# Performance work log

Hardware: AMD Instinct MI355X
Metric: run time of the kernel (lower is better)

Reference implementation:

```python
import jax, jax.numpy as jnp
import numpy as np

B, S, D, N = 8, 4096, 1024, 64
SHIFT_FRAC = 0.5
LN_EPS = 1e-5


def setup_inputs() -> dict:
    key = jax.random.key(0)
    ks = jax.random.split(key, 6)
    x = jax.random.normal(ks[0], (B, S, D), jnp.float32)
    # decay in (-1, 0] so w = exp(decay) in (e^-1, 1] -- stable recurrence
    time_decay = -jax.random.uniform(ks[1], (N,), jnp.float32)
    time_first = 0.1 * jax.random.normal(ks[2], (N,), jnp.float32)
    key_w = jax.random.normal(ks[3], (N, D), jnp.float32) / np.float32(np.sqrt(D))
    value_w = jax.random.normal(ks[4], (N, D), jnp.float32) / np.float32(np.sqrt(D))
    output_w = jax.random.normal(ks[5], (D, N), jnp.float32) / np.float32(np.sqrt(N))
    time_shift_gates = jnp.ones((D,), jnp.float32)
    ln_w = jnp.ones((D,), jnp.float32)
    ln_b = jnp.zeros((D,), jnp.float32)
    return dict(x=x, time_decay=time_decay, time_first=time_first,
                key_w=key_w, value_w=value_w, output_w=output_w,
                time_shift_gates=time_shift_gates, ln_w=ln_w, ln_b=ln_b)


def reference(x, time_decay, time_first, key_w, value_w, output_w,
              time_shift_gates, ln_w, ln_b):
    b, s, d = x.shape
    # ---- token shift (blend current token with shifted sequence) ----
    shift = max(1, int(s * SHIFT_FRAC))
    x_cat = jnp.concatenate([x[:, shift:, :], x[:, :-shift, :]], axis=1)  # (b,s,d)
    g = jax.nn.sigmoid(time_shift_gates)
    x_shift = x_cat * g + x * (1.0 - g)
    # ---- LayerNorm (biased variance, eps=1e-5, affine) ----
    mu = jnp.mean(x_shift, axis=-1, keepdims=True)
    var = jnp.mean((x_shift - mu) ** 2, axis=-1, keepdims=True)
    x_norm = (x_shift - mu) * jax.lax.rsqrt(var + LN_EPS) * ln_w + ln_b
    # ---- K/V projections, batched over all timesteps ----
    k = jnp.einsum('bsd,nd->bsn', x_norm, key_w)   # (b,s,N)
    v = jnp.einsum('bsd,nd->bsn', x_norm, value_w)  # (b,s,N)
    w = jnp.exp(time_decay)                          # (N,)
    wkv = jnp.exp(-jnp.exp(time_first) * k) * v      # (b,s,N)
    # ---- sequential linear recurrence: states = states*w + wkv_t ----
    def step(states, wkv_t):
        states = states * w + wkv_t
        return states, states
    init = jnp.zeros((b, wkv.shape[-1]), x.dtype)
    last_states, states_seq = jax.lax.scan(step, init, jnp.swapaxes(wkv, 0, 1))  # (s,b,N)
    # ---- output projection batched outside the loop ----
    output = jnp.einsum('sbn,dn->bsd', states_seq, output_w)  # (b,s,d)
    # dropout is identity in eval mode
    return output, last_states
```

## Files before the change

kernel.cpp:

```cpp
#include <hip/hip_runtime.h>
#include <math.h>

#define B_ 8
#define S_ 4096
#define D_ 1024
#define N_ 64
#define SHIFT_ 2048
#define LCH 32
#define CCH 128
#define MTOT (B_*S_)
#define EPS_ 1e-5f

typedef __attribute__((ext_vector_type(8))) short v8s;
typedef __attribute__((ext_vector_type(4))) float v4f;

static __device__ __forceinline__ short f2bf(float f) {
    unsigned int u = __float_as_uint(f);
    u += 0x7fffu + ((u >> 16) & 1u);
    return (short)(u >> 16);
}

static __device__ __forceinline__ void gl_lds16(const void* g, void* l) {
    __builtin_amdgcn_global_load_lds(
        (const __attribute__((address_space(1))) unsigned int*)g,
        (__attribute__((address_space(3))) unsigned int*)l,
        16, 0, 0);
}

__global__ __launch_bounds__(256) void k_conv(
    const float* __restrict__ keyw, const float* __restrict__ valw,
    const float* __restrict__ ow, const float* __restrict__ tf,
    const float* __restrict__ tsg,
    short* __restrict__ wbf, short* __restrict__ owbf,
    float* __restrict__ etf, float* __restrict__ g) {
    int i = blockIdx.x * 256 + threadIdx.x;
    if (i < 65536)          wbf[i] = f2bf(keyw[i]);
    else if (i < 131072)    wbf[i] = f2bf(valw[i - 65536]);
    else if (i < 196608)    owbf[i - 131072] = f2bf(ow[i - 131072]);
    else if (i < 196672)    etf[i - 196608] = __expf(tf[i - 196608]);
    else if (i < 197696) {
        int j = i - 196672;
        g[j] = 1.0f / (1.0f + __expf(-tsg[j]));
    }
}

__global__ __launch_bounds__(256) void k_stats_fused(
    const float* __restrict__ x, const float* __restrict__ g,
    const float* __restrict__ lnw, const float* __restrict__ lnb,
    short* __restrict__ xn) {
    int b = blockIdx.x >> 11;
    int t = blockIdx.x & 2047;
    const float* rowa = x + ((size_t)(b * S_ + t)) * D_;
    const float* rowb = rowa + (size_t)SHIFT_ * D_;
    int c = threadIdx.x * 4;
    float4 xa = *(const float4*)(rowa + c);
    float4 xb = *(const float4*)(rowb + c);
    float4 gg = *(const float4*)(g + c);
    float av[4] = {xa.x, xa.y, xa.z, xa.w};
    float bv[4] = {xb.x, xb.y, xb.z, xb.w};
    float gv[4] = {gg.x, gg.y, gg.z, gg.w};
    float u[4], w2[4];
    float s1 = 0.f, q1 = 0.f, s2 = 0.f, q2 = 0.f;
#pragma unroll
    for (int j = 0; j < 4; j++) {
        u[j]  = gv[j] * bv[j] + (1.f - gv[j]) * av[j];
        w2[j] = gv[j] * av[j] + (1.f - gv[j]) * bv[j];
        s1 += u[j];  q1 += u[j] * u[j];
        s2 += w2[j]; q2 += w2[j] * w2[j];
    }
    __shared__ float red[4][4];
    int lane = threadIdx.x & 63, wv = threadIdx.x >> 6;
#pragma unroll
    for (int off = 32; off > 0; off >>= 1) {
        s1 += __shfl_down(s1, off);
        q1 += __shfl_down(q1, off);
        s2 += __shfl_down(s2, off);
        q2 += __shfl_down(q2, off);
    }
    if (lane == 0) { red[wv][0] = s1; red[wv][1] = q1; red[wv][2] = s2; red[wv][3] = q2; }
    __syncthreads();
    float S1 = red[0][0] + red[1][0] + red[2][0] + red[3][0];
    float Q1 = red[0][1] + red[1][1] + red[2][1] + red[3][1];
    float S2 = red[0][2] + red[1][2] + red[2][2] + red[3][2];
    float Q2 = red[0][3] + red[1][3] + red[2][3] + red[3][3];
    float m1 = S1 * (1.f / D_), m2 = S2 * (1.f / D_);
    float rs1 = rsqrtf(Q1 * (1.f / D_) - m1 * m1 + EPS_);
    float rs2 = rsqrtf(Q2 * (1.f / D_) - m2 * m2 + EPS_);
    float4 lw = *(const float4*)(lnw + c);
    float4 lb = *(const float4*)(lnb + c);
    float lwv[4] = {lw.x, lw.y, lw.z, lw.w};
    float lbv[4] = {lb.x, lb.y, lb.z, lb.w};
    short o1[4], o2[4];
#pragma unroll
    for (int j = 0; j < 4; j++) {
        o1[j] = f2bf((u[j]  - m1) * rs1 * lwv[j] + lbv[j]);
        o2[j] = f2bf((w2[j] - m2) * rs2 * lwv[j] + lbv[j]);
    }
    short* d1 = xn + ((size_t)(b * S_ + t)) * D_ + c;
    short* d2 = d1 + (size_t)SHIFT_ * D_;
    *(short4*)d1 = make_short4(o1[0], o1[1], o1[2], o1[3]);
    *(short4*)d2 = make_short4(o2[0], o2[1], o2[2], o2[3]);
}

__global__ __launch_bounds__(256) void k_proj_mx(
    const short* __restrict__ xn, const short* __restrict__ wbf,
    const float* __restrict__ etf, const float* __restrict__ tdec,
    float* __restrict__ wkv, float* __restrict__ Acar) {
    __shared__ __align__(16) char lds[49152];
    char* Ab = lds;
    char* Bb = lds + 16384;
    float* C = (float*)lds;

    int tid = threadIdx.x, wid = tid >> 6, lane = tid & 63;
    int wm = wid >> 1, wn = wid & 1;
    int quad = lane >> 4, l15 = lane & 15;
    int m0 = blockIdx.x * 64;

    const char* xb = (const char*)(xn + (size_t)m0 * D_);
    const char* wb = (const char*)wbf;

    v4f acc[2][4];
#pragma unroll
    for (int i = 0; i < 2; i++)
#pragma unroll
        for (int j = 0; j < 4; j++) acc[i][j] = (v4f)0.f;

    auto stage = [&](int buf, int k0) {
#pragma unroll
        for (int j = 0; j < 2; ++j) {
            int s = j * 256 + wid * 64 + lane;
            int r = s >> 3, cu = s & 7;
            gl_lds16(xb + (size_t)r * 2048 + k0 * 2 + ((cu ^ (r & 7)) << 4),
                     Ab + buf * 8192 + (j * 256 + wid * 64) * 16);
        }
#pragma unroll
        for (int j = 0; j < 4; ++j) {
            int s = j * 256 + wid * 64 + lane;
            int r = s >> 3, cu = s & 7;
            gl_lds16(wb + (size_t)r * 2048 + k0 * 2 + ((cu ^ (r & 7)) << 4),
                     Bb + buf * 16384 + (j * 256 + wid * 64) * 16);
        }
    };
    auto ldA = [&](int buf, int r, int cu) -> v8s {
        return *(const v8s*)(Ab + buf * 8192 + r * 128 + ((cu ^ (r & 7)) << 4));
    };
    auto ldB = [&](int buf, int r, int cu) -> v8s {
        return *(const v8s*)(Bb + buf * 16384 + r * 128 + ((cu ^ (r & 7)) << 4));
    };

    stage(0, 0);
    int cur = 0;
    for (int kt = 0; kt < 16; ++kt) {
        __syncthreads();
        if (kt < 15) stage(cur ^ 1, (kt + 1) * 64);
#pragma unroll
        for (int kk2 = 0; kk2 < 2; ++kk2) {
            int cu = kk2 * 4 + quad;
            v8s a0 = ldA(cur, wm * 32 + l15, cu);
            v8s a1 = ldA(cur, wm * 32 + 16 + l15, cu);
            v8s b0 = ldB(cur, wn * 64 + l15, cu);
            v8s b1 = ldB(cur, wn * 64 + 16 + l15, cu);
            v8s b2 = ldB(cur, wn * 64 + 32 + l15, cu);
            v8s b3 = ldB(cur, wn * 64 + 48 + l15, cu);
            acc[0][0] = __builtin_amdgcn_mfma_f32_16x16x32_bf16(a0, b0, acc[0][0], 0, 0, 0);
            acc[0][1] = __builtin_amdgcn_mfma_f32_16x16x32_bf16(a0, b1, acc[0][1], 0, 0, 0);
            acc[0][2] = __builtin_amdgcn_mfma_f32_16x16x32_bf16(a0, b2, acc[0][2], 0, 0, 0);
            acc[0][3] = __builtin_amdgcn_mfma_f32_16x16x32_bf16(a0, b3, acc[0][3], 0, 0, 0);
            acc[1][0] = __builtin_amdgcn_mfma_f32_16x16x32_bf16(a1, b0, acc[1][0], 0, 0, 0);
            acc[1][1] = __builtin_amdgcn_mfma_f32_16x16x32_bf16(a1, b1, acc[1][1], 0, 0, 0);
            acc[1][2] = __builtin_amdgcn_mfma_f32_16x16x32_bf16(a1, b2, acc[1][2], 0, 0, 0);
            acc[1][3] = __builtin_amdgcn_mfma_f32_16x16x32_bf16(a1, b3, acc[1][3], 0, 0, 0);
        }
        cur ^= 1;
    }
    __syncthreads();

#pragma unroll
    for (int i = 0; i < 2; i++)
#pragma unroll
        for (int j = 0; j < 4; j++)
#pragma unroll
            for (int r = 0; r < 4; r++)
                C[(wm * 32 + i * 16 + quad * 4 + r) * 132 + wn * 64 + j * 16 + l15] = acc[i][j][r];
    __syncthreads();

    int tok = tid >> 2, n0 = (tid & 3) * 16;
    float* orow = wkv + ((size_t)(m0 + tok)) * N_ + n0;
    float os[16];
#pragma unroll
    for (int jj = 0; jj < 16; jj++) {
        float kv = C[tok * 132 + n0 + jj];
        float vv = C[tok * 132 + 64 + n0 + jj];
        os[jj] = __expf(-etf[n0 + jj] * kv) * vv;
    }
#pragma unroll
    for (int jj = 0; jj < 16; jj += 4)
        *(float4*)(orow + jj) = make_float4(os[jj], os[jj + 1], os[jj + 2], os[jj + 3]);
#pragma unroll
    for (int jj = 0; jj < 16; jj++) C[tok * 132 + n0 + jj] = os[jj];
    __syncthreads();

    if (tid < 128) {
        int c = tid >> 6, n = tid & 63;
        float w = expf(tdec[n]);
        float s = 0.f;
#pragma unroll
        for (int i = 0; i < LCH; i++) s = s * w + C[(c * 32 + i) * 132 + n];
        Acar[((size_t)blockIdx.x * 2 + c) * N_ + n] = s;
    }
}

__global__ __launch_bounds__(256) void k_stats_mu(const float* __restrict__ x,
                                                  const float* __restrict__ g,
                                                  float* __restrict__ mu,
                                                  float* __restrict__ rstd) {
    int b = blockIdx.x >> 11;
    int t = blockIdx.x & 2047;
    const float* rowa = x + ((size_t)(b * S_ + t)) * D_;
    const float* rowb = rowa + (size_t)SHIFT_ * D_;
    int c = threadIdx.x * 4;
    float4 xa = *(const float4*)(rowa + c);
    float4 xb = *(const float4*)(rowb + c);
    float4 gg = *(const float4*)(g + c);
    float av[4] = {xa.x, xa.y, xa.z, xa.w};
    float bv[4] = {xb.x, xb.y, xb.z, xb.w};
    float gv[4] = {gg.x, gg.y, gg.z, gg.w};
    float s1 = 0.f, q1 = 0.f, s2 = 0.f, q2 = 0.f;
#pragma unroll
    for (int j = 0; j < 4; j++) {
        float u  = gv[j] * bv[j] + (1.f - gv[j]) * av[j];
        float w2 = gv[j] * av[j] + (1.f - gv[j]) * bv[j];
        s1 += u;  q1 += u * u;
        s2 += w2; q2 += w2 * w2;
    }
    __shared__ float red[4][4];
    int lane = threadIdx.x & 63, wv = threadIdx.x >> 6;
#pragma unroll
    for (int off = 32; off > 0; off >>= 1) {
        s1 += __shfl_down(s1, off);
        q1 += __shfl_down(q1, off);
        s2 += __shfl_down(s2, off);
        q2 += __shfl_down(q2, off);
    }
    if (lane == 0) { red[wv][0] = s1; red[wv][1] = q1; red[wv][2] = s2; red[wv][3] = q2; }
    __syncthreads();
    if (threadIdx.x == 0) {
        float S1 = 0, Q1 = 0, S2 = 0, Q2 = 0;
#pragma unroll
        for (int i = 0; i < 4; i++) { S1 += red[i][0]; Q1 += red[i][1]; S2 += red[i][2]; Q2 += red[i][3]; }
        float m1 = S1 * (1.f / D_), m2 = S2 * (1.f / D_);
        float v1 = Q1 * (1.f / D_) - m1 * m1;
        float v2 = Q2 * (1.f / D_) - m2 * m2;
        int m = b * S_ + t;
        mu[m] = m1;           rstd[m] = rsqrtf(v1 + EPS_);
        mu[m + SHIFT_] = m2;  rstd[m + SHIFT_] = rsqrtf(v2 + EPS_);
    }
}

__global__ __launch_bounds__(256) void k_proj_fp32(
    const float* __restrict__ x, const float* __restrict__ keyw,
    const float* __restrict__ valw, const float* __restrict__ g,
    const float* __restrict__ lnw, const float* __restrict__ lnb,
    const float* __restrict__ tf, const float* __restrict__ mu,
    const float* __restrict__ rstd, float* __restrict__ wkv) {
    __shared__ float smem[64 * 132];
    float* As = smem;
    float* Bs = smem + 64 * 36;

    int m0 = blockIdx.x * 64;
    int b = m0 >> 12;
    int t0 = m0 & 4095;
    int t2 = (t0 + SHIFT_) & 4095;
    const float* xa_base = x + ((size_t)(b * S_ + t0)) * D_;
    const float* xb_base = x + ((size_t)(b * S_ + t2)) * D_;

    int tid = threadIdx.x;
    int ty = tid >> 4, tx = tid & 15;
    int tokA = tid >> 3;
    int cA = (tid & 7) * 4;

    float mu0 = mu[m0 + tokA],      rs0 = rstd[m0 + tokA];
    float mu1 = mu[m0 + tokA + 32], rs1 = rstd[m0 + tokA + 32];

    int nB = tid >> 1;
    int halfB = tid & 1;
    const float* wrow = (nB < 64) ? (keyw + (size_t)nB * D_)
                                  : (valw + (size_t)(nB - 64) * D_);

    float acc[4][8];
#pragma unroll
    for (int i = 0; i < 4; i++)
#pragma unroll
        for (int j = 0; j < 8; j++) acc[i][j] = 0.f;

    for (int kk0 = 0; kk0 < D_; kk0 += 32) {
        float4 gg = *(const float4*)(g + kk0 + cA);
        float4 lw = *(const float4*)(lnw + kk0 + cA);
        float4 lb = *(const float4*)(lnb + kk0 + cA);
        float gv[4] = {gg.x, gg.y, gg.z, gg.w};
        float lwv[4] = {lw.x, lw.y, lw.z, lw.w};
        float lbv[4] = {lb.x, lb.y, lb.z, lb.w};
#pragma unroll
        for (int r = 0; r < 2; r++) {
            int tok = tokA + r * 32;
            float4 xa = *(const float4*)(xa_base + (size_t)tok * D_ + kk0 + cA);
            float4 xb = *(const float4*)(xb_base + (size_t)tok * D_ + kk0 + cA);
            float xav[4] = {xa.x, xa.y, xa.z, xa.w};
            float xbv[4] = {xb.x, xb.y, xb.z, xb.w};
            float m_ = r ? mu1 : mu0;
            float rs_ = r ? rs1 : rs0;
#pragma unroll
            for (int j = 0; j < 4; j++) {
                float xs = gv[j] * xbv[j] + (1.f - gv[j]) * xav[j];
                As[tok * 36 + cA + j] = (xs - m_) * rs_ * lwv[j] + lbv[j];
            }
        }
#pragma unroll
        for (int cc = 0; cc < 16; cc += 4) {
            int kk = halfB * 16 + cc;
            float4 wv4 = *(const float4*)(wrow + kk0 + kk);
            Bs[(kk + 0) * 132 + nB] = wv4.x;
            Bs[(kk + 1) * 132 + nB] = wv4.y;
            Bs[(kk + 2) * 132 + nB] = wv4.z;
            Bs[(kk + 3) * 132 + nB] = wv4.w;
        }
        __syncthreads();
#pragma unroll
        for (int kk = 0; kk < 32; kk++) {
            float a0 = As[(ty * 4 + 0) * 36 + kk];
            float a1 = As[(ty * 4 + 1) * 36 + kk];
            float a2 = As[(ty * 4 + 2) * 36 + kk];
            float a3 = As[(ty * 4 + 3) * 36 + kk];
            float bvv[8];
#pragma unroll
            for (int j = 0; j < 8; j++) bvv[j] = Bs[kk * 132 + tx * 8 + j];
#pragma unroll
            for (int j = 0; j < 8; j++) {
                acc[0][j] = fmaf(a0, bvv[j], acc[0][j]);
                acc[1][j] = fmaf(a1, bvv[j], acc[1][j]);
                acc[2][j] = fmaf(a2, bvv[j], acc[2][j]);
                acc[3][j] = fmaf(a3, bvv[j], acc[3][j]);
            }
        }
        __syncthreads();
    }
#pragma unroll
    for (int i = 0; i < 4; i++)
#pragma unroll
        for (int j = 0; j < 8; j++)
            smem[(ty * 4 + i) * 132 + tx * 8 + j] = acc[i][j];
    __syncthreads();
    {
        int tok = tid >> 2;
        int n0 = (tid & 3) * 16;
        float* orow = wkv + ((size_t)(m0 + tok)) * N_ + n0;
#pragma unroll
        for (int jj = 0; jj < 16; jj++) {
            int n = n0 + jj;
            float kv = smem[tok * 132 + n];
            float vv = smem[tok * 132 + 64 + n];
            orow[jj] = __expf(-__expf(tf[n]) * kv) * vv;
        }
    }
}

__global__ __launch_bounds__(64) void k_chunk(const float* __restrict__ wkv,
                                              const float* __restrict__ tdec,
                                              float* __restrict__ Acar) {
    int idx = blockIdx.x;
    int n = threadIdx.x;
    float w = expf(tdec[n]);
    const float* p = wkv + (size_t)idx * (LCH * N_) + n;
    float s = 0.f;
#pragma unroll
    for (int i = 0; i < LCH; i++) s = s * w + p[i * N_];
    Acar[idx * N_ + n] = s;
}

__global__ __launch_bounds__(64) void k_carry(const float* __restrict__ Acar,
                                              const float* __restrict__ tdec,
                                              float* __restrict__ Cin,
                                              float* __restrict__ last) {
    int b = blockIdx.x;
    int n = threadIdx.x;
    float wL = expf(tdec[n] * (float)LCH);
    float c = 0.f;
#pragma unroll 16
    for (int ch = 0; ch < CCH; ch++) {
        Cin[(b * CCH + ch) * N_ + n] = c;
        c = c * wL + Acar[(b * CCH + ch) * N_ + n];
    }
    last[b * N_ + n] = c;
}

__global__ __launch_bounds__(64) void k_rescan(const float* __restrict__ wkv,
                                               const float* __restrict__ Cin,
                                               const float* __restrict__ tdec,
                                               short* __restrict__ st) {
    int idx = blockIdx.x;
    int n = threadIdx.x;
    float w = expf(tdec[n]);
    float s = Cin[idx * N_ + n];
    const float* p = wkv + (size_t)idx * (LCH * N_) + n;
    short* q = st + (size_t)idx * (LCH * N_) + n;
#pragma unroll
    for (int i = 0; i < LCH; i++) { s = s * w + p[i * N_]; q[i * N_] = f2bf(s); }
}

__global__ __launch_bounds__(256) void k_out_mx(const short* __restrict__ st,
                                                const short* __restrict__ owbf,
                                                float* __restrict__ out) {
    __shared__ float C[64 * 132];
    int tid = threadIdx.x, wid = tid >> 6, lane = tid & 63;
    int wm = wid >> 1, wn = wid & 1;
    int quad = lane >> 4, l15 = lane & 15;
    int m0 = (blockIdx.x >> 3) * 64;
    int d0 = (blockIdx.x & 7) * 128;
    const short* ab = st + ((size_t)(m0 + wm * 32 + l15)) * N_ + quad * 8;
    const short* bb = owbf + ((size_t)(d0 + wn * 64 + l15)) * N_ + quad * 8;
    v4f acc[2][4];
#pragma unroll
    for (int i = 0; i < 2; i++)
#pragma unroll
        for (int j = 0; j < 4; j++) acc[i][j] = (v4f)0.f;
#pragma unroll
    for (int ks = 0; ks < 2; ks++) {
        v8s a0 = *(const v8s*)(ab + ks * 32);
        v8s a1 = *(const v8s*)(ab + 16 * N_ + ks * 32);
        v8s b0 = *(const v8s*)(bb + ks * 32);
        v8s b1 = *(const v8s*)(bb + 16 * N_ + ks * 32);
        v8s b2 = *(const v8s*)(bb + 32 * N_ + ks * 32);
        v8s b3 = *(const v8s*)(bb + 48 * N_ + ks * 32);
        acc[0][0] = __builtin_amdgcn_mfma_f32_16x16x32_bf16(a0, b0, acc[0][0], 0, 0, 0);
        acc[0][1] = __builtin_amdgcn_mfma_f32_16x16x32_bf16(a0, b1, acc[0][1], 0, 0, 0);
        acc[0][2] = __builtin_amdgcn_mfma_f32_16x16x32_bf16(a0, b2, acc[0][2], 0, 0, 0);
        acc[0][3] = __builtin_amdgcn_mfma_f32_16x16x32_bf16(a0, b3, acc[0][3], 0, 0, 0);
        acc[1][0] = __builtin_amdgcn_mfma_f32_16x16x32_bf16(a1, b0, acc[1][0], 0, 0, 0);
        acc[1][1] = __builtin_amdgcn_mfma_f32_16x16x32_bf16(a1, b1, acc[1][1], 0, 0, 0);
        acc[1][2] = __builtin_amdgcn_mfma_f32_16x16x32_bf16(a1, b2, acc[1][2], 0, 0, 0);
        acc[1][3] = __builtin_amdgcn_mfma_f32_16x16x32_bf16(a1, b3, acc[1][3], 0, 0, 0);
    }
#pragma unroll
    for (int i = 0; i < 2; i++)
#pragma unroll
        for (int j = 0; j < 4; j++)
#pragma unroll
            for (int r = 0; r < 4; r++)
                C[(wm * 32 + i * 16 + quad * 4 + r) * 132 + wn * 64 + j * 16 + l15] = acc[i][j][r];
    __syncthreads();
    int rrow = tid >> 3;
    int ccol = (tid & 7) * 4;
#pragma unroll
    for (int rep = 0; rep < 2; rep++) {
        int row = rep * 32 + rrow;
        float* orow = out + ((size_t)(m0 + row)) * D_ + d0;
        const float* crow = &C[row * 132];
#pragma unroll
        for (int k = 0; k < 4; k++) {
            int col = ccol + k * 32;
            *(float4*)(orow + col) = *(const float4*)(crow + col);
        }
    }
}

extern "C" void kernel_launch(void* const* d_in, const int* in_sizes, int n_in,
                              void* d_out, int out_size, void* d_ws, size_t ws_size,
                              hipStream_t stream) {
    const float* x    = (const float*)d_in[0];
    const float* tdec = (const float*)d_in[1];
    const float* tf   = (const float*)d_in[2];
    const float* keyw = (const float*)d_in[3];
    const float* valw = (const float*)d_in[4];
    const float* ow   = (const float*)d_in[5];
    const float* tsg  = (const float*)d_in[6];
    const float* lnw  = (const float*)d_in[7];
    const float* lnb  = (const float*)d_in[8];
    float* out = (float*)d_out;
    float* ws  = (float*)d_ws;

    float* g     = ws;
    float* etf   = g + 1024;
    short* wbf   = (short*)(etf + 64);
    short* owbf  = (short*)(ws + 66624);
    float* mu    = ws + 99392;
    float* rstd  = mu + 32768;
    float* wkv   = rstd + 32768;
    float* Acar  = wkv + 2097152;
    float* Cin   = Acar + 65536;
    short* stbf  = (short*)(Cin + 65536);
    short* xnorm = (short*)(ws + 3441728);
    const size_t NEED_PRIMARY = (size_t)(3441728 + 16777216) * 4;

    k_conv<<<773, 256, 0, stream>>>(keyw, valw, ow, tf, tsg, wbf, owbf, etf, g);

    if (ws_size >= NEED_PRIMARY) {
        k_stats_fused<<<B_ * (S_ / 2), 256, 0, stream>>>(x, g, lnw, lnb, xnorm);
        k_proj_mx<<<MTOT / 64, 256, 0, stream>>>(xnorm, wbf, etf, tdec, wkv, Acar);
    } else {
        k_stats_mu<<<B_ * (S_ / 2), 256, 0, stream>>>(x, g, mu, rstd);
        k_proj_fp32<<<MTOT / 64, 256, 0, stream>>>(x, keyw, valw, g, lnw, lnb, tf, mu, rstd, wkv);
        k_chunk <<<B_ * CCH, 64, 0, stream>>>(wkv, tdec, Acar);
    }
    k_carry <<<B_, 64, 0, stream>>>(Acar, tdec, Cin, out + (size_t)MTOT * D_);
    k_rescan<<<B_ * CCH, 64, 0, stream>>>(wkv, Cin, tdec, stbf);
    k_out_mx<<<(MTOT / 64) * 8, 256, 0, stream>>>(stbf, owbf, out);
}
```

Baseline: 288.9 us.

## Fuse chunk rescan into output projection kernel with LDS-staged states

Removes the separate rescan kernel. The output GEMM kernel now recomputes the per-chunk recurrence from wkv and the carry-in, then writes bf16 states into a swizzled LDS tile and loads its A fragments once. Each block now covers four 128-wide D tiles instead of one, so the A operand is reused, the grid is a quarter the size, and the bf16 state buffer no longer round-trips through global memory. In exchange, the blocks on each 64-row tile redundantly recompute the recurrence, only 128 threads do serial scan work, and each D tile adds barriers.

```diff
diff --git a/kernel.cpp b/kernel.cpp
--- a/kernel.cpp
+++ b/kernel.cpp
@@ -393,72 +393,92 @@
     last[b * N_ + n] = c;
 }
 
-__global__ __launch_bounds__(64) void k_rescan(const float* __restrict__ wkv,
-                                               const float* __restrict__ Cin,
-                                               const float* __restrict__ tdec,
-                                               short* __restrict__ st) {
-    int idx = blockIdx.x;
-    int n = threadIdx.x;
-    float w = expf(tdec[n]);
-    float s = Cin[idx * N_ + n];
-    const float* p = wkv + (size_t)idx * (LCH * N_) + n;
-    short* q = st + (size_t)idx * (LCH * N_) + n;
-#pragma unroll
-    for (int i = 0; i < LCH; i++) { s = s * w + p[i * N_]; q[i * N_] = f2bf(s); }
-}
-
-__global__ __launch_bounds__(256) void k_out_mx(const short* __restrict__ st,
+__global__ __launch_bounds__(256) void k_out_mx(const float* __restrict__ wkv,
+                                                const float* __restrict__ Cin,
+                                                const float* __restrict__ tdec,
                                                 const short* __restrict__ owbf,
                                                 float* __restrict__ out) {
-    __shared__ float C[64 * 132];
+    __shared__ __align__(16) char smem[64 * 132 * 4];
+    char* stl = smem;
+    float* C = (float*)smem;
+
     int tid = threadIdx.x, wid = tid >> 6, lane = tid & 63;
     int wm = wid >> 1, wn = wid & 1;
     int quad = lane >> 4, l15 = lane & 15;
-    int m0 = (blockIdx.x >> 3) * 64;
-    int d0 = (blockIdx.x & 7) * 128;
-    const short* ab = st + ((size_t)(m0 + wm * 32 + l15)) * N_ + quad * 8;
-    const short* bb = owbf + ((size_t)(d0 + wn * 64 + l15)) * N_ + quad * 8;
-    v4f acc[2][4];
+    int m0 = (blockIdx.x >> 1) * 64;
+    int dh = blockIdx.x & 1;
+
+    if (tid < 128) {
+        int c = tid >> 6, n = tid & 63;
+        int idx = (blockIdx.x >> 1) * 2 + c;
+        float w = expf(tdec[n]);
+        float s = Cin[idx * N_ + n];
+        const float* p = wkv + (size_t)idx * (LCH * N_) + n;
+        int cu = (n * 2) >> 4, off = (n * 2) & 15;
+#pragma unroll
+        for (int i = 0; i < LCH; i++) {
+            s = s * w + p[i * N_];
+            int row = c * 32 + i;
+            *(short*)(stl + row * 128 + ((cu ^ (row & 7)) << 4) + off) = f2bf(s);
+        }
+    }
+    __syncthreads();
+
+    v8s a[2][2];
 #pragma unroll
     for (int i = 0; i < 2; i++)
 #pragma unroll
-        for (int j = 0; j < 4; j++) acc[i][j] = (v4f)0.f;
-#pragma unroll
-    for (int ks = 0; ks < 2; ks++) {
-        v8s a0 = *(const v8s*)(ab + ks * 32);
-        v8s a1 = *(const v8s*)(ab + 16 * N_ + ks * 32);
-        v8s b0 = *(const v8s*)(bb + ks * 32);
-        v8s b1 = *(const v8s*)(bb + 16 * N_ + ks * 32);
-        v8s b2 = *(const v8s*)(bb + 32 * N_ + ks * 32);
-        v8s b3 = *(const v8s*)(bb + 48 * N_ + ks * 32);
-        acc[0][0] = __builtin_amdgcn_mfma_f32_16x16x32_bf16(a0, b0, acc[0][0], 0, 0, 0);
-        acc[0][1] = __builtin_amdgcn_mfma_f32_16x16x32_bf16(a0, b1, acc[0][1], 0, 0, 0);
-        acc[0][2] = __builtin_amdgcn_mfma_f32_16x16x32_bf16(a0, b2, acc[0][2], 0, 0, 0);
-        acc[0][3] = __builtin_amdgcn_mfma_f32_16x16x32_bf16(a0, b3, acc[0][3], 0, 0, 0);
-        acc[1][0] = __builtin_amdgcn_mfma_f32_16x16x32_bf16(a1, b0, acc[1][0], 0, 0, 0);
-        acc[1][1] = __builtin_amdgcn_mfma_f32_16x16x32_bf16(a1, b1, acc[1][1], 0, 0, 0);
-        acc[1][2] = __builtin_amdgcn_mfma_f32_16x16x32_bf16(a1, b2, acc[1][2], 0, 0, 0);
-        acc[1][3] = __builtin_amdgcn_mfma_f32_16x16x32_bf16(a1, b3, acc[1][3], 0, 0, 0);
-    }
-#pragma unroll
-    for (int i = 0; i < 2; i++)
-#pragma unroll
-        for (int j = 0; j < 4; j++)
-#pragma unroll
-            for (int r = 0; r < 4; r++)
-                C[(wm * 32 + i * 16 + quad * 4 + r) * 132 + wn * 64 + j * 16 + l15] = acc[i][j][r];
-    __syncthreads();
+        for (int ks = 0; ks < 2; ks++) {
+            int row = wm * 32 + i * 16 + l15;
+            int cu = quad + ks * 4;
+            a[i][ks] = *(const v8s*)(stl + row * 128 + ((cu ^ (row & 7)) << 4));
+        }
+
     int rrow = tid >> 3;
     int ccol = (tid & 7) * 4;
-#pragma unroll
-    for (int rep = 0; rep < 2; rep++) {
-        int row = rep * 32 + rrow;
-        float* orow = out + ((size_t)(m0 + row)) * D_ + d0;
-        const float* crow = &C[row * 132];
-#pragma unroll
-        for (int k = 0; k < 4; k++) {
-            int col = ccol + k * 32;
-            *(float4*)(orow + col) = *(const float4*)(crow + col);
+
+    for (int dt = 0; dt < 4; ++dt) {
+        int d0 = (dh * 4 + dt) * 128;
+        const short* bb = owbf + ((size_t)(d0 + wn * 64 + l15)) * N_ + quad * 8;
+        v4f acc[2][4];
+#pragma unroll
+        for (int i = 0; i < 2; i++)
+#pragma unroll
+            for (int j = 0; j < 4; j++) acc[i][j] = (v4f)0.f;
+#pragma unroll
+        for (int ks = 0; ks < 2; ks++) {
+            v8s b0 = *(const v8s*)(bb + ks * 32);
+            v8s b1 = *(const v8s*)(bb + 16 * N_ + ks * 32);
+            v8s b2 = *(const v8s*)(bb + 32 * N_ + ks * 32);
+            v8s b3 = *(const v8s*)(bb + 48 * N_ + ks * 32);
+            acc[0][0] = __builtin_amdgcn_mfma_f32_16x16x32_bf16(a[0][ks], b0, acc[0][0], 0, 0, 0);
+            acc[0][1] = __builtin_amdgcn_mfma_f32_16x16x32_bf16(a[0][ks], b1, acc[0][1], 0, 0, 0);
+            acc[0][2] = __builtin_amdgcn_mfma_f32_16x16x32_bf16(a[0][ks], b2, acc[0][2], 0, 0, 0);
+            acc[0][3] = __builtin_amdgcn_mfma_f32_16x16x32_bf16(a[0][ks], b3, acc[0][3], 0, 0, 0);
+            acc[1][0] = __builtin_amdgcn_mfma_f32_16x16x32_bf16(a[1][ks], b0, acc[1][0], 0, 0, 0);
+            acc[1][1] = __builtin_amdgcn_mfma_f32_16x16x32_bf16(a[1][ks], b1, acc[1][1], 0, 0, 0);
+            acc[1][2] = __builtin_amdgcn_mfma_f32_16x16x32_bf16(a[1][ks], b2, acc[1][2], 0, 0, 0);
+            acc[1][3] = __builtin_amdgcn_mfma_f32_16x16x32_bf16(a[1][ks], b3, acc[1][3], 0, 0, 0);
+        }
+        __syncthreads();
+#pragma unroll
+        for (int i = 0; i < 2; i++)
+#pragma unroll
+            for (int j = 0; j < 4; j++)
+#pragma unroll
+                for (int r = 0; r < 4; r++)
+                    C[(wm * 32 + i * 16 + quad * 4 + r) * 132 + wn * 64 + j * 16 + l15] = acc[i][j][r];
+        __syncthreads();
+#pragma unroll
+        for (int rep = 0; rep < 2; rep++) {
+            int row = rep * 32 + rrow;
+            float* orow = out + ((size_t)(m0 + row)) * D_ + d0;
+            const float* crow = &C[row * 132];
+#pragma unroll
+            for (int k = 0; k < 4; k++) {
+                int col = ccol + k * 32;
+                *(float4*)(orow + col) = *(const float4*)(crow + col);
+            }
         }
     }
 }
@@ -487,7 +507,6 @@
     float* wkv   = rstd + 32768;
     float* Acar  = wkv + 2097152;
     float* Cin   = Acar + 65536;
-    short* stbf  = (short*)(Cin + 65536);
     short* xnorm = (short*)(ws + 3441728);
     const size_t NEED_PRIMARY = (size_t)(3441728 + 16777216) * 4;
 
@@ -502,6 +521,5 @@
         k_chunk <<<B_ * CCH, 64, 0, stream>>>(wkv, tdec, Acar);
     }
     k_carry <<<B_, 64, 0, stream>>>(Acar, tdec, Cin, out + (size_t)MTOT * D_);
-    k_rescan<<<B_ * CCH, 64, 0, stream>>>(wkv, Cin, tdec, stbf);
-    k_out_mx<<<(MTOT / 64) * 8, 256, 0, stream>>>(stbf, owbf, out);
-}
+    k_out_mx<<<(MTOT / 64) * 2, 256, 0, stream>>>(wkv, Cin, tdec, owbf, out);
+}
```

Result: no change. 291.4 us (+0.9%).
